# Kernel tuning notes

Measured on AMD Instinct MI355X. Metric: run time of the kernel, lower is better.

The kernel has to match this reference:

```python
import jax, jax.numpy as jnp
import numpy as np
import math

NUM_HEADS = 16
D_MODEL = 1024
BATCH = 1
SEQ_LEN = 4096


def alibi_slopes(num_heads):
    # slopes m_h = (256 ** (1/H)) ** -(h+1)
    x = (2.0 ** 8) ** (1.0 / num_heads)
    return jnp.asarray([1.0 / x ** (i + 1) for i in range(num_heads)], dtype=jnp.float32)


def setup_inputs() -> dict:
    key = jax.random.key(0)
    k1, k2 = jax.random.split(key)
    x = jax.random.normal(k1, (BATCH, SEQ_LEN, D_MODEL), dtype=jnp.float32)
    # nn.Linear(d_model, 3*d_model, bias=False); store as [d_model, 3*d_model] so y = x @ w
    w_kqv = jax.random.normal(k2, (D_MODEL, 3 * D_MODEL), dtype=jnp.float32) * (1.0 / math.sqrt(D_MODEL))
    return {"x": x, "w_kqv": w_kqv}


def reference(x, w_kqv):
    B, S, D = x.shape
    H = NUM_HEADS
    dh = D // H
    scale = jnp.asarray(math.sqrt(D), dtype=x.dtype)  # module divides by sqrt(d_model)

    kqv = x @ w_kqv  # [B, S, 3D]
    # NOTE: original chunks as (key, query, value) in that order
    k, q, v = jnp.split(kqv, 3, axis=-1)
    q = q.reshape(B, S, H, dh)
    k = k.reshape(B, S, H, dh)
    v = v.reshape(B, S, H, dh)

    # ALiBi bias: m_h * (j - i), shape [H, S, S]
    pos = jnp.arange(S)
    rel = pos[None, :] - pos[:, None]  # [S, S], x - y
    slopes = alibi_slopes(H).astype(x.dtype)  # [H]
    bias = slopes[:, None, None] * rel.astype(x.dtype)  # [H, S, S]

    score = jnp.einsum('bihd,bjhd->bhij', q, k) / scale + bias[None]  # [B, H, S, S]
    causal = rel <= 0  # j <= i (lower triangular)
    score = jnp.where(causal[None, None], score, jnp.asarray(-jnp.inf, dtype=score.dtype))

    attn = jax.nn.softmax(score, axis=-1)
    out = jnp.einsum('bhij,bjhd->bihd', attn, v).reshape(B, S, D)
    return out
```

## Files before the change

### kernel.cpp

```cpp
#include <hip/hip_runtime.h>
#include <stdint.h>
#include <math.h>

#define SEQ 4096
#define DM  1024
#define NH  16
#define DH  64
#define PPAD 72
#define LOG2E 1.44269504088896341f

typedef short bf16x8 __attribute__((ext_vector_type(8)));
typedef short bf16x4 __attribute__((ext_vector_type(4)));
typedef float f32x4  __attribute__((ext_vector_type(4)));

typedef const __attribute__((address_space(1))) short* gptr_t;
typedef __attribute__((address_space(3))) short* lptr_t;

__device__ __forceinline__ short f2bf(float f) {
    union { float f; uint32_t u; } x; x.f = f;
    uint32_t r = (x.u + 0x7fffu + ((x.u >> 16) & 1u)) >> 16;
    return (short)r;
}
__device__ __forceinline__ short f2bf_trunc(float f) {
    union { float f; uint32_t u; } x; x.f = f;
    return (short)(x.u >> 16);
}

__device__ __forceinline__ void load_lds16(const short* g, const short* l) {
    __builtin_amdgcn_global_load_lds((gptr_t)(uintptr_t)g,
                                     (lptr_t)(uint32_t)(uintptr_t)l, 16, 0, 0);
}

__global__ __launch_bounds__(256) void cvt_fused(const float* __restrict__ x,
                                                 const float* __restrict__ w,
                                                 short* __restrict__ xb,
                                                 short* __restrict__ wtb) {
    __shared__ float T[64][69];
    const int b = blockIdx.x;
    if (b < 2048) {
        const int i = (b * 256 + threadIdx.x) * 8;
        float4 a0 = ((const float4*)(x + i))[0];
        float4 a1 = ((const float4*)(x + i))[1];
        bf16x8 p;
        p[0]=f2bf(a0.x); p[1]=f2bf(a0.y); p[2]=f2bf(a0.z); p[3]=f2bf(a0.w);
        p[4]=f2bf(a1.x); p[5]=f2bf(a1.y); p[6]=f2bf(a1.z); p[7]=f2bf(a1.w);
        *(bf16x8*)(xb + i) = p;
        return;
    }
    const int bb = b - 2048;
    const int n0 = (bb % 48) * 64, k0 = (bb / 48) * 64;
    const int t = threadIdx.x;
    {
        const int kr = t >> 4, nc = (t & 15) * 4;
        #pragma unroll
        for (int i = 0; i < 4; ++i) {
            float4 v = *(const float4*)(w + (size_t)(k0 + kr + i * 16) * 3072 + n0 + nc);
            T[kr + i * 16][nc + 0] = v.x; T[kr + i * 16][nc + 1] = v.y;
            T[kr + i * 16][nc + 2] = v.z; T[kr + i * 16][nc + 3] = v.w;
        }
    }
    __syncthreads();
    const int nr = t >> 4, kc = (t & 15) * 4;
    #pragma unroll
    for (int i = 0; i < 4; ++i) {
        const int n = n0 + nr + i * 16;
        const float sc = (n >= 1024 && n < 2048) ? (LOG2E / 32.0f) : 1.0f;
        short4 o;
        o.x = f2bf(T[kc + 0][nr + i * 16] * sc);
        o.y = f2bf(T[kc + 1][nr + i * 16] * sc);
        o.z = f2bf(T[kc + 2][nr + i * 16] * sc);
        o.w = f2bf(T[kc + 3][nr + i * 16] * sc);
        *(short4*)(wtb + (size_t)n * 1024 + k0 + kc) = o;
    }
}

__global__ __launch_bounds__(256) void qkv_gemm(const short* __restrict__ xb,
                                                const short* __restrict__ wtb,
                                                short* __restrict__ kq,
                                                short* __restrict__ vt) {
    __shared__ short As[128 * 64];
    __shared__ short Bs[128 * 64];
    const int col0 = blockIdx.y * 128, row0 = blockIdx.x * 128;
    const int tid = threadIdx.x, w = tid >> 6, lane = tid & 63;
    const int lmod = lane & 15, ldiv = lane >> 4;
    const int wr = (w >> 1) * 64, wc = (w & 1) * 64;

    f32x4 acc[4][4] = {};
    const short* Ag = xb  + (size_t)row0 * DM;
    const short* Bg = wtb + (size_t)col0 * DM;

    for (int k0 = 0; k0 < DM; k0 += 64) {
        __syncthreads();
        #pragma unroll
        for (int t = 0; t < 4; ++t) {
            const int o = (w * 4 + t) * 1024 + lane * 16;
            const int r = o >> 7, cs = (o & 127) >> 1;
            load_lds16(Ag + (size_t)r * DM + k0 + cs, As + (w * 4 + t) * 512);
            load_lds16(Bg + (size_t)r * DM + k0 + cs, Bs + (w * 4 + t) * 512);
        }
        __syncthreads();
        #pragma unroll
        for (int ks = 0; ks < 2; ++ks) {
            bf16x8 af[4], bf[4];
            #pragma unroll
            for (int i = 0; i < 4; ++i)
                af[i] = *(const bf16x8*)(As + (wr + i * 16 + lmod) * 64 + ks * 32 + ldiv * 8);
            #pragma unroll
            for (int j = 0; j < 4; ++j)
                bf[j] = *(const bf16x8*)(Bs + (wc + j * 16 + lmod) * 64 + ks * 32 + ldiv * 8);
            #pragma unroll
            for (int i = 0; i < 4; ++i)
                #pragma unroll
                for (int j = 0; j < 4; ++j)
                    acc[i][j] = __builtin_amdgcn_mfma_f32_16x16x32_bf16(af[i], bf[j], acc[i][j], 0, 0, 0);
        }
    }

    if (col0 < 2048) {
        #pragma unroll
        for (int i = 0; i < 4; ++i)
            #pragma unroll
            for (int j = 0; j < 4; ++j)
                #pragma unroll
                for (int r = 0; r < 4; ++r)
                    kq[(size_t)(row0 + wr + i * 16 + ldiv * 4 + r) * 2048
                       + col0 + wc + j * 16 + lmod] = f2bf(acc[i][j][r]);
    } else {
        #pragma unroll
        for (int i = 0; i < 4; ++i) {
            const int ig = row0 + wr + i * 16 + ldiv * 4;
            #pragma unroll
            for (int j = 0; j < 4; ++j) {
                const int cg = col0 + wc + j * 16 + lmod - 2048;
                const int h = cg >> 6, d = cg & 63;
                bf16x4 p;
                p[0]=f2bf(acc[i][j][0]); p[1]=f2bf(acc[i][j][1]);
                p[2]=f2bf(acc[i][j][2]); p[3]=f2bf(acc[i][j][3]);
                *(bf16x4*)(vt + (size_t)(h * 64 + d) * SEQ + ig) = p;
            }
        }
    }
}

__global__ __launch_bounds__(256, 4) void attn(const short* __restrict__ kq,
                                               const short* __restrict__ vt,
                                               float* __restrict__ o0,
                                               float* __restrict__ o1,
                                               float* __restrict__ ls0,
                                               float* __restrict__ ls1) {
    __shared__ short Ks[64 * 64];
    __shared__ short Vs[64 * 64];
    __shared__ short Ps[4 * 32 * PPAD];

    const int b = blockIdx.x;
    const int band = b >> 8, pos = b & 255, g = pos >> 5;
    const int qt = (band & 1) ? (24 - band * 8 + g) : (31 - band * 8 - g);
    const int h = (pos >> 1) & 15, s = pos & 1;

    const int tid = threadIdx.x, w = tid >> 6, lane = tid & 63;
    const int lmod = lane & 15, ldiv = lane >> 4;
    const float slope2 = exp2f(-0.5f * (float)(h + 1)) * LOG2E;

    const int sr0 = w * 16 + (lane >> 3), sr1 = sr0 + 8;
    const int sc0 = (lane & 7) ^ (sr0 & 7), sc1 = (lane & 7) ^ (sr1 & 7);

    const int xorm = lmod & 7;
    const int cx0 = ldiv ^ xorm;
    const int cx1 = (4 + ldiv) ^ xorm;
    const int rowbase = qt * 128 + w * 32;
    short* pw = Ps + w * 32 * PPAD;

    bf16x8 qf[2][2];
    #pragma unroll
    for (int m = 0; m < 2; ++m) {
        const short* qp = kq + (size_t)(rowbase + m * 16 + lmod) * 2048 + 1024 + h * 64;
        qf[m][0] = *(const bf16x8*)(qp + ldiv * 8);
        qf[m][1] = *(const bf16x8*)(qp + 32 + ldiv * 8);
    }
    int db[2];
    float pre[2][4];
    #pragma unroll
    for (int m = 0; m < 2; ++m) {
        db[m] = lmod - (rowbase + m * 16 + ldiv * 4);
        #pragma unroll
        for (int r = 0; r < 4; ++r) pre[m][r] = slope2 * (float)(db[m] - r);
    }

    f32x4 O[2][4] = {};
    float lsum[2][4] = {};
    const int kt0 = s ? (qt + 1) : 0;
    const int kt1 = s ? (2 * qt + 2) : (qt + 1);

    for (int kt = kt0; kt < kt1; ++kt) {
        __syncthreads();
        {
            const short* kb = kq + (size_t)(kt * 64) * 2048 + h * 64;
            load_lds16(kb + (size_t)sr0 * 2048 + sc0 * 8, Ks + (w * 16) * 64);
            load_lds16(kb + (size_t)sr1 * 2048 + sc1 * 8, Ks + (w * 16 + 8) * 64);
            const short* vb = vt + (size_t)(h * 64) * SEQ + kt * 64;
            load_lds16(vb + (size_t)sr0 * SEQ + sc0 * 8, Vs + (w * 16) * 64);
            load_lds16(vb + (size_t)sr1 * SEQ + sc1 * 8, Vs + (w * 16 + 8) * 64);
        }
        __syncthreads();

        const bool diag = (kt >= 2 * qt);
        const float cb = slope2 * (float)(kt * 64);
        const int dt = kt * 64;

        #pragma unroll
        for (int nt = 0; nt < 4; ++nt) {
            const float cn = cb + slope2 * (float)(nt * 16);
            f32x4 sc[2];
            #pragma unroll
            for (int m = 0; m < 2; ++m)
                #pragma unroll
                for (int r = 0; r < 4; ++r) sc[m][r] = pre[m][r] + cn;
            #pragma unroll
            for (int ks = 0; ks < 2; ++ks) {
                bf16x8 kf = *(const bf16x8*)(Ks + (nt * 16 + lmod) * 64 + ((ks ? cx1 : cx0) << 3));
                #pragma unroll
                for (int m = 0; m < 2; ++m)
                    sc[m] = __builtin_amdgcn_mfma_f32_16x16x32_bf16(qf[m][ks], kf, sc[m], 0, 0, 0);
            }
            if (diag) {
                #pragma unroll
                for (int m = 0; m < 2; ++m)
                    #pragma unroll
                    for (int r = 0; r < 4; ++r) {
                        float v = sc[m][r];
                        if (dt + nt * 16 - r + db[m] > 0) v = -1e30f;
                        const float p = __builtin_amdgcn_exp2f(v);
                        lsum[m][r] += p;
                        pw[(m * 16 + ldiv * 4 + r) * PPAD + nt * 16 + lmod] = f2bf_trunc(p);
                    }
            } else {
                #pragma unroll
                for (int m = 0; m < 2; ++m)
                    #pragma unroll
                    for (int r = 0; r < 4; ++r) {
                        const float p = __builtin_amdgcn_exp2f(sc[m][r]);
                        lsum[m][r] += p;
                        pw[(m * 16 + ldiv * 4 + r) * PPAD + nt * 16 + lmod] = f2bf_trunc(p);
                    }
            }
        }

        bf16x8 pa[2][2];
        #pragma unroll
        for (int m = 0; m < 2; ++m) {
            pa[m][0] = *(const bf16x8*)(pw + (m * 16 + lmod) * PPAD + ldiv * 8);
            pa[m][1] = *(const bf16x8*)(pw + (m * 16 + lmod) * PPAD + 32 + ldiv * 8);
        }
        #pragma unroll
        for (int ks = 0; ks < 2; ++ks) {
            const int cxo = (ks ? cx1 : cx0) << 3;
            #pragma unroll
            for (int nt = 0; nt < 4; ++nt) {
                bf16x8 vf = *(const bf16x8*)(Vs + (nt * 16 + lmod) * 64 + cxo);
                #pragma unroll
                for (int m = 0; m < 2; ++m)
                    O[m][nt] = __builtin_amdgcn_mfma_f32_16x16x32_bf16(pa[m][ks], vf, O[m][nt], 0, 0, 0);
            }
        }
    }

    #pragma unroll
    for (int m = 0; m < 2; ++m)
        #pragma unroll
        for (int r = 0; r < 4; ++r) {
            float v = lsum[m][r];
            v += __shfl_xor(v, 1, 16);
            v += __shfl_xor(v, 2, 16);
            v += __shfl_xor(v, 4, 16);
            v += __shfl_xor(v, 8, 16);
            lsum[m][r] = v;
        }

    float* ob = s ? o1 : o0;
    float* lb = s ? ls1 : ls0;
    #pragma unroll
    for (int m = 0; m < 2; ++m) {
        const int i0 = rowbase + m * 16 + ldiv * 4;
        #pragma unroll
        for (int nt = 0; nt < 4; ++nt)
            #pragma unroll
            for (int r = 0; r < 4; ++r)
                ob[(size_t)(i0 + r) * DM + h * 64 + nt * 16 + lmod] = O[m][nt][r];
    }
    if (lmod == 0) {
        #pragma unroll
        for (int m = 0; m < 2; ++m)
            #pragma unroll
            for (int r = 0; r < 4; ++r)
                lb[h * SEQ + rowbase + m * 16 + ldiv * 4 + r] = lsum[m][r];
    }
}

__global__ __launch_bounds__(256) void combine(float* __restrict__ out,
                                               const float* __restrict__ opart,
                                               const float* __restrict__ ls0,
                                               const float* __restrict__ ls1) {
    const int i8 = (blockIdx.x * 256 + threadIdx.x) * 8;
    const int row = i8 >> 10, col = i8 & 1023, h = col >> 6;
    const float l = ls0[h * SEQ + row] + ls1[h * SEQ + row];
    const float rc = 1.0f / l;
    float4 a0 = *(const float4*)(out + i8);
    float4 a1 = *(const float4*)(out + i8 + 4);
    float4 b0 = *(const float4*)(opart + i8);
    float4 b1 = *(const float4*)(opart + i8 + 4);
    float4 c0, c1;
    c0.x = (a0.x + b0.x) * rc; c0.y = (a0.y + b0.y) * rc;
    c0.z = (a0.z + b0.z) * rc; c0.w = (a0.w + b0.w) * rc;
    c1.x = (a1.x + b1.x) * rc; c1.y = (a1.y + b1.y) * rc;
    c1.z = (a1.z + b1.z) * rc; c1.w = (a1.w + b1.w) * rc;
    *(float4*)(out + i8) = c0;
    *(float4*)(out + i8 + 4) = c1;
}

extern "C" void kernel_launch(void* const* d_in, const int* in_sizes, int n_in,
                              void* d_out, int out_size, void* d_ws, size_t ws_size,
                              hipStream_t stream) {
    const float* x = (const float*)d_in[0];
    const float* w = (const float*)d_in[1];
    float* out = (float*)d_out;

    char* ws = (char*)d_ws;
    short* kq    = (short*)(ws);
    short* vt    = (short*)(ws + ((size_t)16 << 20));
    short* xb    = (short*)(ws + ((size_t)24 << 20));
    short* wtb   = (short*)(ws + ((size_t)32 << 20));
    float* opart = (float*)(ws + ((size_t)24 << 20));
    float* ls0   = (float*)(ws + ((size_t)40 << 20));
    float* ls1   = (float*)(ws + ((size_t)40 << 20) + (256 << 10));

    cvt_fused<<<2048 + 768, 256, 0, stream>>>(x, w, xb, wtb);
    qkv_gemm <<<dim3(SEQ / 128, 3072 / 128), 256, 0, stream>>>(xb, wtb, kq, vt);
    attn     <<<1024, 256, 0, stream>>>(kq, vt, out, opart, ls0, ls1);
    combine  <<<SEQ * DM / (256 * 8), 256, 0, stream>>>(out, opart, ls0, ls1);
}
```

Before: 191.2 us.

## Split attention key range four ways with atomic accumulation and transposed score MFMA

The attention grid changes from a fixed two-way split over balanced bands to a four-way even split of each query tile's causal key range (2048 blocks). Partial outputs and row sums now go into a zeroed workspace through float atomics instead of two separate partial buffers. The score MFMA operands are swapped so each lane owns a query row, which lets P be packed as bf16x4 stores and the row-sum reduction shrink to two shuffles. This adds a memset and heavy fp32 atomic traffic on the output, and drops the earlier interleaved tile ordering used for load balance.

```diff
diff --git a/kernel.cpp b/kernel.cpp
--- a/kernel.cpp
+++ b/kernel.cpp
@@ -6,7 +6,7 @@
 #define DM  1024
 #define NH  16
 #define DH  64
-#define PPAD 72
+#define PSTR 72
 #define LOG2E 1.44269504088896341f
 
 typedef short bf16x8 __attribute__((ext_vector_type(8)));
@@ -21,9 +21,8 @@
     uint32_t r = (x.u + 0x7fffu + ((x.u >> 16) & 1u)) >> 16;
     return (short)r;
 }
-__device__ __forceinline__ short f2bf_trunc(float f) {
-    union { float f; uint32_t u; } x; x.f = f;
-    return (short)(x.u >> 16);
+__device__ __forceinline__ uint32_t fbits(float f) {
+    union { float f; uint32_t u; } x; x.f = f; return x.u;
 }
 
 __device__ __forceinline__ void load_lds16(const short* g, const short* l) {
@@ -144,18 +143,18 @@
 
 __global__ __launch_bounds__(256, 4) void attn(const short* __restrict__ kq,
                                                const short* __restrict__ vt,
-                                               float* __restrict__ o0,
-                                               float* __restrict__ o1,
-                                               float* __restrict__ ls0,
-                                               float* __restrict__ ls1) {
+                                               float* __restrict__ oacc,
+                                               float* __restrict__ ls) {
     __shared__ short Ks[64 * 64];
     __shared__ short Vs[64 * 64];
-    __shared__ short Ps[4 * 32 * PPAD];
+    __shared__ short Ps[4 * 32 * PSTR];
 
     const int b = blockIdx.x;
-    const int band = b >> 8, pos = b & 255, g = pos >> 5;
-    const int qt = (band & 1) ? (24 - band * 8 + g) : (31 - band * 8 - g);
-    const int h = (pos >> 1) & 15, s = pos & 1;
+    const int qt = 31 - (b >> 6);
+    const int h = (b >> 2) & 15, s = b & 3;
+    const int T = 2 * qt + 2;
+    const int c0 = (s * T) >> 2, c1 = ((s + 1) * T) >> 2;
+    if (c0 == c1) return;
 
     const int tid = threadIdx.x, w = tid >> 6, lane = tid & 63;
     const int lmod = lane & 15, ldiv = lane >> 4;
@@ -163,12 +162,11 @@
 
     const int sr0 = w * 16 + (lane >> 3), sr1 = sr0 + 8;
     const int sc0 = (lane & 7) ^ (sr0 & 7), sc1 = (lane & 7) ^ (sr1 & 7);
-
     const int xorm = lmod & 7;
-    const int cx0 = ldiv ^ xorm;
-    const int cx1 = (4 + ldiv) ^ xorm;
+    const int cx0 = ldiv ^ xorm, cx1 = (4 + ldiv) ^ xorm;
+
     const int rowbase = qt * 128 + w * 32;
-    short* pw = Ps + w * 32 * PPAD;
+    short* pw = Ps + w * 32 * PSTR;
 
     bf16x8 qf[2][2];
     #pragma unroll
@@ -177,21 +175,19 @@
         qf[m][0] = *(const bf16x8*)(qp + ldiv * 8);
         qf[m][1] = *(const bf16x8*)(qp + 32 + ldiv * 8);
     }
-    int db[2];
+    int dbI[2];
     float pre[2][4];
     #pragma unroll
-    for (int m = 0; m < 2; ++m) {
-        db[m] = lmod - (rowbase + m * 16 + ldiv * 4);
-        #pragma unroll
-        for (int r = 0; r < 4; ++r) pre[m][r] = slope2 * (float)(db[m] - r);
+    for (int ib = 0; ib < 2; ++ib) {
+        dbI[ib] = ldiv * 4 - rowbase - ib * 16 - lmod;
+        #pragma unroll
+        for (int r = 0; r < 4; ++r) pre[ib][r] = slope2 * (float)(dbI[ib] + r);
     }
 
     f32x4 O[2][4] = {};
-    float lsum[2][4] = {};
-    const int kt0 = s ? (qt + 1) : 0;
-    const int kt1 = s ? (2 * qt + 2) : (qt + 1);
-
-    for (int kt = kt0; kt < kt1; ++kt) {
+    float lsum[2] = {0.f, 0.f};
+
+    for (int kt = c0; kt < c1; ++kt) {
         __syncthreads();
         {
             const short* kb = kq + (size_t)(kt * 64) * 2048 + h * 64;
@@ -204,52 +200,51 @@
         __syncthreads();
 
         const bool diag = (kt >= 2 * qt);
-        const float cb = slope2 * (float)(kt * 64);
         const int dt = kt * 64;
 
         #pragma unroll
-        for (int nt = 0; nt < 4; ++nt) {
-            const float cn = cb + slope2 * (float)(nt * 16);
+        for (int jb = 0; jb < 4; ++jb) {
+            const float cn = slope2 * (float)(dt + jb * 16);
             f32x4 sc[2];
             #pragma unroll
-            for (int m = 0; m < 2; ++m)
-                #pragma unroll
-                for (int r = 0; r < 4; ++r) sc[m][r] = pre[m][r] + cn;
+            for (int ib = 0; ib < 2; ++ib)
+                #pragma unroll
+                for (int r = 0; r < 4; ++r) sc[ib][r] = pre[ib][r] + cn;
             #pragma unroll
             for (int ks = 0; ks < 2; ++ks) {
-                bf16x8 kf = *(const bf16x8*)(Ks + (nt * 16 + lmod) * 64 + ((ks ? cx1 : cx0) << 3));
-                #pragma unroll
-                for (int m = 0; m < 2; ++m)
-                    sc[m] = __builtin_amdgcn_mfma_f32_16x16x32_bf16(qf[m][ks], kf, sc[m], 0, 0, 0);
+                bf16x8 kf = *(const bf16x8*)(Ks + (jb * 16 + lmod) * 64 + ((ks ? cx1 : cx0) << 3));
+                #pragma unroll
+                for (int ib = 0; ib < 2; ++ib)
+                    sc[ib] = __builtin_amdgcn_mfma_f32_16x16x32_bf16(kf, qf[ib][ks], sc[ib], 0, 0, 0);
             }
-            if (diag) {
-                #pragma unroll
-                for (int m = 0; m < 2; ++m)
-                    #pragma unroll
-                    for (int r = 0; r < 4; ++r) {
-                        float v = sc[m][r];
-                        if (dt + nt * 16 - r + db[m] > 0) v = -1e30f;
-                        const float p = __builtin_amdgcn_exp2f(v);
-                        lsum[m][r] += p;
-                        pw[(m * 16 + ldiv * 4 + r) * PPAD + nt * 16 + lmod] = f2bf_trunc(p);
-                    }
-            } else {
-                #pragma unroll
-                for (int m = 0; m < 2; ++m)
-                    #pragma unroll
-                    for (int r = 0; r < 4; ++r) {
-                        const float p = __builtin_amdgcn_exp2f(sc[m][r]);
-                        lsum[m][r] += p;
-                        pw[(m * 16 + ldiv * 4 + r) * PPAD + nt * 16 + lmod] = f2bf_trunc(p);
-                    }
+            #pragma unroll
+            for (int ib = 0; ib < 2; ++ib) {
+                float p0, p1, p2, p3;
+                if (diag) {
+                    const int dj = dt + jb * 16 + dbI[ib];
+                    p0 = __builtin_amdgcn_exp2f((dj + 0 > 0) ? -1e30f : sc[ib][0]);
+                    p1 = __builtin_amdgcn_exp2f((dj + 1 > 0) ? -1e30f : sc[ib][1]);
+                    p2 = __builtin_amdgcn_exp2f((dj + 2 > 0) ? -1e30f : sc[ib][2]);
+                    p3 = __builtin_amdgcn_exp2f((dj + 3 > 0) ? -1e30f : sc[ib][3]);
+                } else {
+                    p0 = __builtin_amdgcn_exp2f(sc[ib][0]);
+                    p1 = __builtin_amdgcn_exp2f(sc[ib][1]);
+                    p2 = __builtin_amdgcn_exp2f(sc[ib][2]);
+                    p3 = __builtin_amdgcn_exp2f(sc[ib][3]);
+                }
+                lsum[ib] += (p0 + p1) + (p2 + p3);
+                uint2 pk;
+                pk.x = (fbits(p0) >> 16) | (fbits(p1) & 0xFFFF0000u);
+                pk.y = (fbits(p2) >> 16) | (fbits(p3) & 0xFFFF0000u);
+                *(uint2*)(pw + (ib * 16 + lmod) * PSTR + jb * 16 + ldiv * 4) = pk;
             }
         }
 
         bf16x8 pa[2][2];
         #pragma unroll
-        for (int m = 0; m < 2; ++m) {
-            pa[m][0] = *(const bf16x8*)(pw + (m * 16 + lmod) * PPAD + ldiv * 8);
-            pa[m][1] = *(const bf16x8*)(pw + (m * 16 + lmod) * PPAD + 32 + ldiv * 8);
+        for (int ib = 0; ib < 2; ++ib) {
+            pa[ib][0] = *(const bf16x8*)(pw + (ib * 16 + lmod) * PSTR + ldiv * 8);
+            pa[ib][1] = *(const bf16x8*)(pw + (ib * 16 + lmod) * PSTR + 32 + ldiv * 8);
         }
         #pragma unroll
         for (int ks = 0; ks < 2; ++ks) {
@@ -258,61 +253,47 @@
             for (int nt = 0; nt < 4; ++nt) {
                 bf16x8 vf = *(const bf16x8*)(Vs + (nt * 16 + lmod) * 64 + cxo);
                 #pragma unroll
-                for (int m = 0; m < 2; ++m)
-                    O[m][nt] = __builtin_amdgcn_mfma_f32_16x16x32_bf16(pa[m][ks], vf, O[m][nt], 0, 0, 0);
+                for (int ib = 0; ib < 2; ++ib)
+                    O[ib][nt] = __builtin_amdgcn_mfma_f32_16x16x32_bf16(pa[ib][ks], vf, O[ib][nt], 0, 0, 0);
             }
         }
     }
 
     #pragma unroll
-    for (int m = 0; m < 2; ++m)
-        #pragma unroll
-        for (int r = 0; r < 4; ++r) {
-            float v = lsum[m][r];
-            v += __shfl_xor(v, 1, 16);
-            v += __shfl_xor(v, 2, 16);
-            v += __shfl_xor(v, 4, 16);
-            v += __shfl_xor(v, 8, 16);
-            lsum[m][r] = v;
-        }
-
-    float* ob = s ? o1 : o0;
-    float* lb = s ? ls1 : ls0;
-    #pragma unroll
-    for (int m = 0; m < 2; ++m) {
-        const int i0 = rowbase + m * 16 + ldiv * 4;
+    for (int ib = 0; ib < 2; ++ib) {
+        float v = lsum[ib];
+        v += __shfl_xor(v, 16);
+        v += __shfl_xor(v, 32);
+        lsum[ib] = v;
+    }
+    if (ldiv == 0) {
+        #pragma unroll
+        for (int ib = 0; ib < 2; ++ib)
+            unsafeAtomicAdd(&ls[h * SEQ + rowbase + ib * 16 + lmod], lsum[ib]);
+    }
+    #pragma unroll
+    for (int ib = 0; ib < 2; ++ib) {
+        const int i0 = rowbase + ib * 16 + ldiv * 4;
         #pragma unroll
         for (int nt = 0; nt < 4; ++nt)
             #pragma unroll
             for (int r = 0; r < 4; ++r)
-                ob[(size_t)(i0 + r) * DM + h * 64 + nt * 16 + lmod] = O[m][nt][r];
-    }
-    if (lmod == 0) {
-        #pragma unroll
-        for (int m = 0; m < 2; ++m)
-            #pragma unroll
-            for (int r = 0; r < 4; ++r)
-                lb[h * SEQ + rowbase + m * 16 + ldiv * 4 + r] = lsum[m][r];
+                unsafeAtomicAdd(&oacc[(size_t)(i0 + r) * DM + h * 64 + nt * 16 + lmod],
+                                O[ib][nt][r]);
     }
 }
 
 __global__ __launch_bounds__(256) void combine(float* __restrict__ out,
-                                               const float* __restrict__ opart,
-                                               const float* __restrict__ ls0,
-                                               const float* __restrict__ ls1) {
+                                               const float* __restrict__ oacc,
+                                               const float* __restrict__ ls) {
     const int i8 = (blockIdx.x * 256 + threadIdx.x) * 8;
     const int row = i8 >> 10, col = i8 & 1023, h = col >> 6;
-    const float l = ls0[h * SEQ + row] + ls1[h * SEQ + row];
-    const float rc = 1.0f / l;
-    float4 a0 = *(const float4*)(out + i8);
-    float4 a1 = *(const float4*)(out + i8 + 4);
-    float4 b0 = *(const float4*)(opart + i8);
-    float4 b1 = *(const float4*)(opart + i8 + 4);
+    const float rc = 1.0f / ls[h * SEQ + row];
+    float4 a0 = *(const float4*)(oacc + i8);
+    float4 a1 = *(const float4*)(oacc + i8 + 4);
     float4 c0, c1;
-    c0.x = (a0.x + b0.x) * rc; c0.y = (a0.y + b0.y) * rc;
-    c0.z = (a0.z + b0.z) * rc; c0.w = (a0.w + b0.w) * rc;
-    c1.x = (a1.x + b1.x) * rc; c1.y = (a1.y + b1.y) * rc;
-    c1.z = (a1.z + b1.z) * rc; c1.w = (a1.w + b1.w) * rc;
+    c0.x = a0.x * rc; c0.y = a0.y * rc; c0.z = a0.z * rc; c0.w = a0.w * rc;
+    c1.x = a1.x * rc; c1.y = a1.y * rc; c1.z = a1.z * rc; c1.w = a1.w * rc;
     *(float4*)(out + i8) = c0;
     *(float4*)(out + i8 + 4) = c1;
 }
@@ -325,16 +306,16 @@
     float* out = (float*)d_out;
 
     char* ws = (char*)d_ws;
-    short* kq    = (short*)(ws);
-    short* vt    = (short*)(ws + ((size_t)16 << 20));
-    short* xb    = (short*)(ws + ((size_t)24 << 20));
-    short* wtb   = (short*)(ws + ((size_t)32 << 20));
-    float* opart = (float*)(ws + ((size_t)24 << 20));
-    float* ls0   = (float*)(ws + ((size_t)40 << 20));
-    float* ls1   = (float*)(ws + ((size_t)40 << 20) + (256 << 10));
+    short* kq   = (short*)(ws);
+    short* vt   = (short*)(ws + ((size_t)16 << 20));
+    short* xb   = (short*)(ws + ((size_t)24 << 20));
+    short* wtb  = (short*)(ws + ((size_t)32 << 20));
+    float* oacc = (float*)(ws + ((size_t)24 << 20));
+    float* ls   = (float*)(ws + ((size_t)40 << 20));
 
     cvt_fused<<<2048 + 768, 256, 0, stream>>>(x, w, xb, wtb);
     qkv_gemm <<<dim3(SEQ / 128, 3072 / 128), 256, 0, stream>>>(xb, wtb, kq, vt);
-    attn     <<<1024, 256, 0, stream>>>(kq, vt, out, opart, ls0, ls1);
-    combine  <<<SEQ * DM / (256 * 8), 256, 0, stream>>>(out, opart, ls0, ls1);
-}
+    hipMemsetAsync(ws + ((size_t)24 << 20), 0, ((size_t)16 << 20) + (256 << 10), stream);
+    attn     <<<2048, 256, 0, stream>>>(kq, vt, oacc, ls);
+    combine  <<<SEQ * DM / (256 * 8), 256, 0, stream>>>(out, oacc, ls);
+}
```

Result: slower. 223.6 us (+17.0%).

## Rebalance attention work as paired q-tiles split three ways along keys

Applied to the files above, without the earlier changes.

Attention blocks now each process a pair of query tiles (qt and 31-qt) so every block gets equal causal work. Each pair's key range is split into three chunks across 768 blocks instead of 1024 blocks with two-way splits and band ordering. Two of the three partial outputs are stored in bf16 to cut write and read traffic in the combine step, which now sums three partials. This trades fewer blocks and some precision in the partials for better load balance and less memory traffic.

```diff
diff --git a/kernel.cpp b/kernel.cpp
--- a/kernel.cpp
+++ b/kernel.cpp
@@ -24,6 +24,10 @@
 __device__ __forceinline__ short f2bf_trunc(float f) {
     union { float f; uint32_t u; } x; x.f = f;
     return (short)(x.u >> 16);
+}
+__device__ __forceinline__ float bf2f(short s) {
+    union { uint32_t u; float f; } x; x.u = ((uint32_t)(uint16_t)s) << 16;
+    return x.f;
 }
 
 __device__ __forceinline__ void load_lds16(const short* g, const short* l) {
@@ -145,17 +149,16 @@
 __global__ __launch_bounds__(256, 4) void attn(const short* __restrict__ kq,
                                                const short* __restrict__ vt,
                                                float* __restrict__ o0,
-                                               float* __restrict__ o1,
-                                               float* __restrict__ ls0,
-                                               float* __restrict__ ls1) {
+                                               short* __restrict__ p1,
+                                               short* __restrict__ p2,
+                                               float* __restrict__ ls) {
     __shared__ short Ks[64 * 64];
     __shared__ short Vs[64 * 64];
     __shared__ short Ps[4 * 32 * PPAD];
 
     const int b = blockIdx.x;
-    const int band = b >> 8, pos = b & 255, g = pos >> 5;
-    const int qt = (band & 1) ? (24 - band * 8 + g) : (31 - band * 8 - g);
-    const int h = (pos >> 1) & 15, s = pos & 1;
+    const int h = b & 15, u = b >> 4;
+    const int qi = u & 15, s = u >> 4;
 
     const int tid = threadIdx.x, w = tid >> 6, lane = tid & 63;
     const int lmod = lane & 15, ldiv = lane >> 4;
@@ -163,158 +166,176 @@
 
     const int sr0 = w * 16 + (lane >> 3), sr1 = sr0 + 8;
     const int sc0 = (lane & 7) ^ (sr0 & 7), sc1 = (lane & 7) ^ (sr1 & 7);
-
     const int xorm = lmod & 7;
-    const int cx0 = ldiv ^ xorm;
-    const int cx1 = (4 + ldiv) ^ xorm;
-    const int rowbase = qt * 128 + w * 32;
+    const int cx0 = ldiv ^ xorm, cx1 = (4 + ldiv) ^ xorm;
     short* pw = Ps + w * 32 * PPAD;
 
-    bf16x8 qf[2][2];
-    #pragma unroll
-    for (int m = 0; m < 2; ++m) {
-        const short* qp = kq + (size_t)(rowbase + m * 16 + lmod) * 2048 + 1024 + h * 64;
-        qf[m][0] = *(const bf16x8*)(qp + ldiv * 8);
-        qf[m][1] = *(const bf16x8*)(qp + 32 + ldiv * 8);
-    }
-    int db[2];
-    float pre[2][4];
-    #pragma unroll
-    for (int m = 0; m < 2; ++m) {
-        db[m] = lmod - (rowbase + m * 16 + ldiv * 4);
-        #pragma unroll
-        for (int r = 0; r < 4; ++r) pre[m][r] = slope2 * (float)(db[m] - r);
-    }
-
-    f32x4 O[2][4] = {};
-    float lsum[2][4] = {};
-    const int kt0 = s ? (qt + 1) : 0;
-    const int kt1 = s ? (2 * qt + 2) : (qt + 1);
-
-    for (int kt = kt0; kt < kt1; ++kt) {
-        __syncthreads();
-        {
-            const short* kb = kq + (size_t)(kt * 64) * 2048 + h * 64;
-            load_lds16(kb + (size_t)sr0 * 2048 + sc0 * 8, Ks + (w * 16) * 64);
-            load_lds16(kb + (size_t)sr1 * 2048 + sc1 * 8, Ks + (w * 16 + 8) * 64);
-            const short* vb = vt + (size_t)(h * 64) * SEQ + kt * 64;
-            load_lds16(vb + (size_t)sr0 * SEQ + sc0 * 8, Vs + (w * 16) * 64);
-            load_lds16(vb + (size_t)sr1 * SEQ + sc1 * 8, Vs + (w * 16 + 8) * 64);
-        }
-        __syncthreads();
-
-        const bool diag = (kt >= 2 * qt);
-        const float cb = slope2 * (float)(kt * 64);
-        const int dt = kt * 64;
-
-        #pragma unroll
-        for (int nt = 0; nt < 4; ++nt) {
-            const float cn = cb + slope2 * (float)(nt * 16);
-            f32x4 sc[2];
+    for (int side = 0; side < 2; ++side) {
+        const int qt = side ? qi : (31 - qi);
+        const int T = 2 * qt + 2;
+        const int c0 = (s * T) / 3, c1 = ((s + 1) * T) / 3;
+        const int rowbase = qt * 128 + w * 32;
+
+        bf16x8 qf[2][2];
+        #pragma unroll
+        for (int m = 0; m < 2; ++m) {
+            const short* qp = kq + (size_t)(rowbase + m * 16 + lmod) * 2048 + 1024 + h * 64;
+            qf[m][0] = *(const bf16x8*)(qp + ldiv * 8);
+            qf[m][1] = *(const bf16x8*)(qp + 32 + ldiv * 8);
+        }
+        int db[2];
+        float pre[2][4];
+        #pragma unroll
+        for (int m = 0; m < 2; ++m) {
+            db[m] = lmod - (rowbase + m * 16 + ldiv * 4);
+            #pragma unroll
+            for (int r = 0; r < 4; ++r) pre[m][r] = slope2 * (float)(db[m] - r);
+        }
+
+        f32x4 O[2][4] = {};
+        float lsum[2][4] = {};
+
+        for (int kt = c0; kt < c1; ++kt) {
+            __syncthreads();
+            {
+                const short* kb = kq + (size_t)(kt * 64) * 2048 + h * 64;
+                load_lds16(kb + (size_t)sr0 * 2048 + sc0 * 8, Ks + (w * 16) * 64);
+                load_lds16(kb + (size_t)sr1 * 2048 + sc1 * 8, Ks + (w * 16 + 8) * 64);
+                const short* vb = vt + (size_t)(h * 64) * SEQ + kt * 64;
+                load_lds16(vb + (size_t)sr0 * SEQ + sc0 * 8, Vs + (w * 16) * 64);
+                load_lds16(vb + (size_t)sr1 * SEQ + sc1 * 8, Vs + (w * 16 + 8) * 64);
+            }
+            __syncthreads();
+
+            const bool diag = (kt >= 2 * qt);
+            const float cb = slope2 * (float)(kt * 64);
+            const int dt = kt * 64;
+
+            #pragma unroll
+            for (int nt = 0; nt < 4; ++nt) {
+                const float cn = cb + slope2 * (float)(nt * 16);
+                f32x4 sc[2];
+                #pragma unroll
+                for (int m = 0; m < 2; ++m)
+                    #pragma unroll
+                    for (int r = 0; r < 4; ++r) sc[m][r] = pre[m][r] + cn;
+                #pragma unroll
+                for (int ks = 0; ks < 2; ++ks) {
+                    bf16x8 kf = *(const bf16x8*)(Ks + (nt * 16 + lmod) * 64 + ((ks ? cx1 : cx0) << 3));
+                    #pragma unroll
+                    for (int m = 0; m < 2; ++m)
+                        sc[m] = __builtin_amdgcn_mfma_f32_16x16x32_bf16(qf[m][ks], kf, sc[m], 0, 0, 0);
+                }
+                if (diag) {
+                    #pragma unroll
+                    for (int m = 0; m < 2; ++m)
+                        #pragma unroll
+                        for (int r = 0; r < 4; ++r) {
+                            float v = sc[m][r];
+                            if (dt + nt * 16 - r + db[m] > 0) v = -1e30f;
+                            const float p = __builtin_amdgcn_exp2f(v);
+                            lsum[m][r] += p;
+                            pw[(m * 16 + ldiv * 4 + r) * PPAD + nt * 16 + lmod] = f2bf_trunc(p);
+                        }
+                } else {
+                    #pragma unroll
+                    for (int m = 0; m < 2; ++m)
+                        #pragma unroll
+                        for (int r = 0; r < 4; ++r) {
+                            const float p = __builtin_amdgcn_exp2f(sc[m][r]);
+                            lsum[m][r] += p;
+                            pw[(m * 16 + ldiv * 4 + r) * PPAD + nt * 16 + lmod] = f2bf_trunc(p);
+                        }
+                }
+            }
+
+            bf16x8 pa[2][2];
+            #pragma unroll
+            for (int m = 0; m < 2; ++m) {
+                pa[m][0] = *(const bf16x8*)(pw + (m * 16 + lmod) * PPAD + ldiv * 8);
+                pa[m][1] = *(const bf16x8*)(pw + (m * 16 + lmod) * PPAD + 32 + ldiv * 8);
+            }
+            #pragma unroll
+            for (int ks = 0; ks < 2; ++ks) {
+                const int cxo = (ks ? cx1 : cx0) << 3;
+                #pragma unroll
+                for (int nt = 0; nt < 4; ++nt) {
+                    bf16x8 vf = *(const bf16x8*)(Vs + (nt * 16 + lmod) * 64 + cxo);
+                    #pragma unroll
+                    for (int m = 0; m < 2; ++m)
+                        O[m][nt] = __builtin_amdgcn_mfma_f32_16x16x32_bf16(pa[m][ks], vf, O[m][nt], 0, 0, 0);
+                }
+            }
+        }
+
+        #pragma unroll
+        for (int m = 0; m < 2; ++m)
+            #pragma unroll
+            for (int r = 0; r < 4; ++r) {
+                float v = lsum[m][r];
+                v += __shfl_xor(v, 1, 16);
+                v += __shfl_xor(v, 2, 16);
+                v += __shfl_xor(v, 4, 16);
+                v += __shfl_xor(v, 8, 16);
+                lsum[m][r] = v;
+            }
+        if (lmod == 0) {
             #pragma unroll
             for (int m = 0; m < 2; ++m)
                 #pragma unroll
-                for (int r = 0; r < 4; ++r) sc[m][r] = pre[m][r] + cn;
-            #pragma unroll
-            for (int ks = 0; ks < 2; ++ks) {
-                bf16x8 kf = *(const bf16x8*)(Ks + (nt * 16 + lmod) * 64 + ((ks ? cx1 : cx0) << 3));
-                #pragma unroll
-                for (int m = 0; m < 2; ++m)
-                    sc[m] = __builtin_amdgcn_mfma_f32_16x16x32_bf16(qf[m][ks], kf, sc[m], 0, 0, 0);
-            }
-            if (diag) {
-                #pragma unroll
-                for (int m = 0; m < 2; ++m)
-                    #pragma unroll
-                    for (int r = 0; r < 4; ++r) {
-                        float v = sc[m][r];
-                        if (dt + nt * 16 - r + db[m] > 0) v = -1e30f;
-                        const float p = __builtin_amdgcn_exp2f(v);
-                        lsum[m][r] += p;
-                        pw[(m * 16 + ldiv * 4 + r) * PPAD + nt * 16 + lmod] = f2bf_trunc(p);
-                    }
-            } else {
-                #pragma unroll
-                for (int m = 0; m < 2; ++m)
-                    #pragma unroll
-                    for (int r = 0; r < 4; ++r) {
-                        const float p = __builtin_amdgcn_exp2f(sc[m][r]);
-                        lsum[m][r] += p;
-                        pw[(m * 16 + ldiv * 4 + r) * PPAD + nt * 16 + lmod] = f2bf_trunc(p);
-                    }
-            }
-        }
-
-        bf16x8 pa[2][2];
-        #pragma unroll
-        for (int m = 0; m < 2; ++m) {
-            pa[m][0] = *(const bf16x8*)(pw + (m * 16 + lmod) * PPAD + ldiv * 8);
-            pa[m][1] = *(const bf16x8*)(pw + (m * 16 + lmod) * PPAD + 32 + ldiv * 8);
-        }
-        #pragma unroll
-        for (int ks = 0; ks < 2; ++ks) {
-            const int cxo = (ks ? cx1 : cx0) << 3;
-            #pragma unroll
-            for (int nt = 0; nt < 4; ++nt) {
-                bf16x8 vf = *(const bf16x8*)(Vs + (nt * 16 + lmod) * 64 + cxo);
-                #pragma unroll
-                for (int m = 0; m < 2; ++m)
-                    O[m][nt] = __builtin_amdgcn_mfma_f32_16x16x32_bf16(pa[m][ks], vf, O[m][nt], 0, 0, 0);
-            }
-        }
-    }
-
-    #pragma unroll
-    for (int m = 0; m < 2; ++m)
-        #pragma unroll
-        for (int r = 0; r < 4; ++r) {
-            float v = lsum[m][r];
-            v += __shfl_xor(v, 1, 16);
-            v += __shfl_xor(v, 2, 16);
-            v += __shfl_xor(v, 4, 16);
-            v += __shfl_xor(v, 8, 16);
-            lsum[m][r] = v;
-        }
-
-    float* ob = s ? o1 : o0;
-    float* lb = s ? ls1 : ls0;
-    #pragma unroll
-    for (int m = 0; m < 2; ++m) {
-        const int i0 = rowbase + m * 16 + ldiv * 4;
-        #pragma unroll
-        for (int nt = 0; nt < 4; ++nt)
-            #pragma unroll
-            for (int r = 0; r < 4; ++r)
-                ob[(size_t)(i0 + r) * DM + h * 64 + nt * 16 + lmod] = O[m][nt][r];
-    }
-    if (lmod == 0) {
-        #pragma unroll
-        for (int m = 0; m < 2; ++m)
-            #pragma unroll
-            for (int r = 0; r < 4; ++r)
-                lb[h * SEQ + rowbase + m * 16 + ldiv * 4 + r] = lsum[m][r];
+                for (int r = 0; r < 4; ++r)
+                    ls[s * (NH * SEQ) + h * SEQ + rowbase + m * 16 + ldiv * 4 + r] = lsum[m][r];
+        }
+        if (s == 0) {
+            #pragma unroll
+            for (int m = 0; m < 2; ++m) {
+                const int i0 = rowbase + m * 16 + ldiv * 4;
+                #pragma unroll
+                for (int nt = 0; nt < 4; ++nt)
+                    #pragma unroll
+                    for (int r = 0; r < 4; ++r)
+                        o0[(size_t)(i0 + r) * DM + h * 64 + nt * 16 + lmod] = O[m][nt][r];
+            }
+        } else {
+            short* pb = (s == 1) ? p1 : p2;
+            #pragma unroll
+            for (int m = 0; m < 2; ++m) {
+                const int i0 = rowbase + m * 16 + ldiv * 4;
+                #pragma unroll
+                for (int nt = 0; nt < 4; ++nt)
+                    #pragma unroll
+                    for (int r = 0; r < 4; ++r)
+                        pb[(size_t)(i0 + r) * DM + h * 64 + nt * 16 + lmod] = f2bf(O[m][nt][r]);
+            }
+        }
     }
 }
 
 __global__ __launch_bounds__(256) void combine(float* __restrict__ out,
-                                               const float* __restrict__ opart,
-                                               const float* __restrict__ ls0,
-                                               const float* __restrict__ ls1) {
+                                               const float* __restrict__ o0,
+                                               const short* __restrict__ p1,
+                                               const short* __restrict__ p2,
+                                               const float* __restrict__ ls) {
     const int i8 = (blockIdx.x * 256 + threadIdx.x) * 8;
-    const int row = i8 >> 10, col = i8 & 1023, h = col >> 6;
-    const float l = ls0[h * SEQ + row] + ls1[h * SEQ + row];
+    const int row = i8 >> 10, h = (i8 & 1023) >> 6;
+    const int li = h * SEQ + row;
+    const float l = ls[li] + ls[NH * SEQ + li] + ls[2 * NH * SEQ + li];
     const float rc = 1.0f / l;
-    float4 a0 = *(const float4*)(out + i8);
-    float4 a1 = *(const float4*)(out + i8 + 4);
-    float4 b0 = *(const float4*)(opart + i8);
-    float4 b1 = *(const float4*)(opart + i8 + 4);
-    float4 c0, c1;
-    c0.x = (a0.x + b0.x) * rc; c0.y = (a0.y + b0.y) * rc;
-    c0.z = (a0.z + b0.z) * rc; c0.w = (a0.w + b0.w) * rc;
-    c1.x = (a1.x + b1.x) * rc; c1.y = (a1.y + b1.y) * rc;
-    c1.z = (a1.z + b1.z) * rc; c1.w = (a1.w + b1.w) * rc;
-    *(float4*)(out + i8) = c0;
-    *(float4*)(out + i8 + 4) = c1;
+    float4 a0 = *(const float4*)(o0 + i8);
+    float4 a1 = *(const float4*)(o0 + i8 + 4);
+    bf16x8 b = *(const bf16x8*)(p1 + i8);
+    bf16x8 c = *(const bf16x8*)(p2 + i8);
+    float4 r0, r1;
+    r0.x = (a0.x + bf2f(b[0]) + bf2f(c[0])) * rc;
+    r0.y = (a0.y + bf2f(b[1]) + bf2f(c[1])) * rc;
+    r0.z = (a0.z + bf2f(b[2]) + bf2f(c[2])) * rc;
+    r0.w = (a0.w + bf2f(b[3]) + bf2f(c[3])) * rc;
+    r1.x = (a1.x + bf2f(b[4]) + bf2f(c[4])) * rc;
+    r1.y = (a1.y + bf2f(b[5]) + bf2f(c[5])) * rc;
+    r1.z = (a1.z + bf2f(b[6]) + bf2f(c[6])) * rc;
+    r1.w = (a1.w + bf2f(b[7]) + bf2f(c[7])) * rc;
+    *(float4*)(out + i8) = r0;
+    *(float4*)(out + i8 + 4) = r1;
 }
 
 extern "C" void kernel_launch(void* const* d_in, const int* in_sizes, int n_in,
@@ -325,16 +346,16 @@
     float* out = (float*)d_out;
 
     char* ws = (char*)d_ws;
-    short* kq    = (short*)(ws);
-    short* vt    = (short*)(ws + ((size_t)16 << 20));
-    short* xb    = (short*)(ws + ((size_t)24 << 20));
-    short* wtb   = (short*)(ws + ((size_t)32 << 20));
-    float* opart = (float*)(ws + ((size_t)24 << 20));
-    float* ls0   = (float*)(ws + ((size_t)40 << 20));
-    float* ls1   = (float*)(ws + ((size_t)40 << 20) + (256 << 10));
+    short* kq  = (short*)(ws);
+    short* vt  = (short*)(ws + ((size_t)16 << 20));
+    short* xb  = (short*)(ws + ((size_t)24 << 20));
+    short* wtb = (short*)(ws + ((size_t)32 << 20));
+    short* p1  = (short*)(ws + ((size_t)24 << 20));
+    short* p2  = (short*)(ws + ((size_t)32 << 20));
+    float* ls  = (float*)(ws + ((size_t)40 << 20));
 
     cvt_fused<<<2048 + 768, 256, 0, stream>>>(x, w, xb, wtb);
     qkv_gemm <<<dim3(SEQ / 128, 3072 / 128), 256, 0, stream>>>(xb, wtb, kq, vt);
-    attn     <<<1024, 256, 0, stream>>>(kq, vt, out, opart, ls0, ls1);
-    combine  <<<SEQ * DM / (256 * 8), 256, 0, stream>>>(out, opart, ls0, ls1);
-}
+    attn     <<<768, 256, 0, stream>>>(kq, vt, out, p1, p2, ls);
+    combine  <<<SEQ * DM / (256 * 8), 256, 0, stream>>>(out, out, p1, p2, ls);
+}
```

Result: slower. 197.0 us (+3.0%).
